# Optimization experiments

Hardware: AMD Instinct MI355X
Metric: run time of the kernel (lower is better)

The kernel has to match this reference:

```python
import jax, jax.numpy as jnp
import numpy as np

B, HW, ENC, DEC, ATTN = 512, 196, 2048, 512, 512

def setup_inputs() -> dict:
    key = jax.random.key(0)
    ks = jax.random.split(key, 8)
    s_enc = 1.0 / np.sqrt(ENC)
    s_dec = 1.0 / np.sqrt(DEC)
    s_v = 1.0 / np.sqrt(ATTN)
    return {
        "enc_out": jax.random.normal(ks[0], (B, HW, ENC), dtype=jnp.float32),
        "dec_h": jax.random.normal(ks[1], (B, DEC), dtype=jnp.float32),
        "W_enc": jax.random.uniform(ks[2], (ENC, ATTN), jnp.float32, -s_enc, s_enc),
        "b_enc": jax.random.uniform(ks[3], (ATTN,), jnp.float32, -s_enc, s_enc),
        "W_dec": jax.random.uniform(ks[4], (DEC, ATTN), jnp.float32, -s_dec, s_dec),
        "b_dec": jax.random.uniform(ks[5], (ATTN,), jnp.float32, -s_dec, s_dec),
        "W_v": jax.random.uniform(ks[6], (ATTN,), jnp.float32, -s_v, s_v),
        "b_v": jax.random.uniform(ks[7], (), jnp.float32, -s_v, s_v),
    }

def reference(enc_out, dec_h, W_enc, b_enc, W_dec, b_dec, W_v, b_v):
    # attn1: [B, HW, ATTN]; attn2: [B, 1, ATTN]
    attn1 = jnp.einsum('bse,ea->bsa', enc_out, W_enc) + b_enc
    attn2 = (dec_h @ W_dec + b_dec)[:, None, :]
    score = jax.nn.relu(attn1 + attn2)
    logits = jnp.einsum('bsa,a->bs', score, W_v) + b_v  # [B, HW]
    alpha = jax.nn.softmax(logits, axis=1)
    context_vec = jnp.einsum('bs,bse->be', alpha, enc_out)
    return (context_vec, alpha)
```

## Files before the change

kernel.cpp:

```cpp
#include <hip/hip_runtime.h>
#include <hip/hip_bf16.h>
#include <cstdint>
#include <cstddef>

#define B_    512
#define HW_   196
#define ENC_  2048
#define DEC_  512
#define ATTN_ 512
#define M_    (B_*HW_)

typedef __attribute__((ext_vector_type(8))) short short8;
typedef __attribute__((ext_vector_type(4))) float f32x4;

__device__ __forceinline__ unsigned short f2bf(float x) {
  __bf16 b = (__bf16)x;
  return __builtin_bit_cast(unsigned short, b);
}
__device__ __forceinline__ unsigned int cvt2(float x, float y) {
  return (unsigned)f2bf(x) | ((unsigned)f2bf(y) << 16);
}

__device__ __forceinline__ void gload_lds16(const void* g, void* l) {
  __builtin_amdgcn_global_load_lds(
      (const __attribute__((address_space(1))) void*)g,
      (__attribute__((address_space(3))) void*)l, 16, 0, 0);
}

__device__ __forceinline__ int invswz8(int p) {
  const int b2 = ((p >> 2) ^ (p >> 4)) & 1;
  const int b1 = ((p >> 1) ^ (p >> 3)) & 1;
  const int b0 = (p ^ (p >> 2) ^ (p >> 4)) & 1;
  return (p & ~7) | (b2 << 2) | (b1 << 1) | b0;
}

__global__ __launch_bounds__(256)
void k_attn2(const float* __restrict__ dec_h, const float* __restrict__ Wdec,
             const float* __restrict__ bdec, const float* __restrict__ benc,
             float* __restrict__ attn2p) {
  __shared__ float dh[DEC_];
  const int b = blockIdx.x;
  const int t = threadIdx.x;
  dh[t]       = dec_h[b*DEC_ + t];
  dh[t + 256] = dec_h[b*DEC_ + t + 256];
  __syncthreads();
  #pragma unroll
  for (int rep = 0; rep < 2; ++rep) {
    const int a = t + rep*256;
    float acc = bdec[a] + benc[a];
    #pragma unroll 8
    for (int k = 0; k < DEC_; ++k)
      acc = fmaf(dh[k], Wdec[(size_t)k*ATTN_ + a], acc);
    attn2p[(size_t)b*ATTN_ + a] = acc;
  }
}

__global__ __launch_bounds__(256)
void k_transpose(const float* __restrict__ Wenc, unsigned short* __restrict__ WencT) {
  __shared__ float tile[32][33];
  const int e0 = blockIdx.x * 32;
  const int a0 = blockIdx.y * 32;
  const int t  = threadIdx.x;
  const int li = t >> 5;
  const int lj = t & 31;
  #pragma unroll
  for (int rep = 0; rep < 4; ++rep) {
    const int i = li + rep*8;
    tile[i][lj] = Wenc[(size_t)(e0 + i)*ATTN_ + a0 + lj];
  }
  __syncthreads();
  #pragma unroll
  for (int rep = 0; rep < 4; ++rep) {
    const int ar = li + rep*8;
    WencT[(size_t)(a0 + ar)*ENC_ + e0 + lj] = f2bf(tile[lj][ar]);
  }
}

#define BM 128
#define BN 128
#define BK 32
#define LDA 40
#define NT (ENC_/BK)

__global__ __launch_bounds__(256)
void k_gemm_logits(const float* __restrict__ enc,
                   const unsigned short* __restrict__ WencT,
                   const float* __restrict__ attn2p,
                   const float* __restrict__ Wv,
                   float* __restrict__ partials) {
  __shared__ unsigned short As[BM*LDA];
  __shared__ unsigned short Bs[2][BN*BK];
  __shared__ float plog[BM][2];

  const int tid  = threadIdx.x;
  const int id   = blockIdx.x;
  const int xcd  = id & 7;
  const int rest = id >> 3;
  const int nb   = rest & 3;
  const int mblk = (rest >> 2) * 8 + xcd;
  const int r0 = mblk * BM;
  const int n0 = nb * BN;

  const int arow  = tid >> 1;
  const int ahalf = (tid & 1) << 4;
  const float* aptr = enc + (size_t)(r0 + arow)*ENC_ + ahalf;

  const unsigned short* bbase = WencT + (size_t)n0*ENC_;

  const int w  = tid >> 6;
  const int l  = tid & 63;
  const int wm = w >> 1, wn = w & 1;
  const int lrow = l & 15;
  const int kg   = l >> 4;
  const int lk8  = kg << 3;
  const int g4   = kg << 2;

  f32x4 acc[4][4];
  #pragma unroll
  for (int mi = 0; mi < 4; ++mi)
    #pragma unroll
    for (int ni = 0; ni < 4; ++ni)
      acc[mi][ni] = (f32x4){0.f, 0.f, 0.f, 0.f};

  float4 ar[4];
  #pragma unroll
  for (int i = 0; i < 4; ++i) ar[i] = *reinterpret_cast<const float4*>(aptr + i*4);
  #pragma unroll
  for (int r = 0; r < 2; ++r) {
    const int p = r*256 + tid;
    const int c = invswz8(p);
    gload_lds16(bbase + (size_t)(c >> 2)*ENC_ + (c & 3)*8, &Bs[0][p*8]);
  }

  for (int kt = 0; kt < NT; ++kt) {
    {
      unsigned int pk[8];
      #pragma unroll
      for (int i = 0; i < 4; ++i) {
        pk[2*i]   = cvt2(ar[i].x, ar[i].y);
        pk[2*i+1] = cvt2(ar[i].z, ar[i].w);
      }
      uint4* da = reinterpret_cast<uint4*>(&As[arow*LDA + ahalf]);
      da[0] = make_uint4(pk[0], pk[1], pk[2], pk[3]);
      da[1] = make_uint4(pk[4], pk[5], pk[6], pk[7]);
    }
    __syncthreads();

    if (kt + 1 < NT) {
      const float* ap = aptr + (kt + 1)*BK;
      #pragma unroll
      for (int i = 0; i < 4; ++i) ar[i] = *reinterpret_cast<const float4*>(ap + i*4);
      const int k0n = (kt + 1)*BK;
      unsigned short* bdst = Bs[(kt + 1) & 1];
      #pragma unroll
      for (int r = 0; r < 2; ++r) {
        const int p = r*256 + tid;
        const int c = invswz8(p);
        gload_lds16(bbase + (size_t)(c >> 2)*ENC_ + k0n + (c & 3)*8, &bdst[p*8]);
      }
    }

    const unsigned short* bsc = Bs[kt & 1];
    short8 aF[4], bF[4];
    #pragma unroll
    for (int mi = 0; mi < 4; ++mi)
      aF[mi] = *reinterpret_cast<const short8*>(&As[(wm*64 + mi*16 + lrow)*LDA + lk8]);
    #pragma unroll
    for (int ni = 0; ni < 4; ++ni) {
      const int cr = ((wn*64 + ni*16 + lrow) << 2) + kg;
      const int pr = cr ^ ((cr >> 2) & 7);
      bF[ni] = *reinterpret_cast<const short8*>(&bsc[pr << 3]);
    }
    #pragma unroll
    for (int mi = 0; mi < 4; ++mi)
      #pragma unroll
      for (int ni = 0; ni < 4; ++ni)
        acc[mi][ni] = __builtin_amdgcn_mfma_f32_16x16x32_bf16(aF[mi], bF[ni], acc[mi][ni], 0, 0, 0);
    __syncthreads();
  }

  float wvv[4];
  #pragma unroll
  for (int ni = 0; ni < 4; ++ni) wvv[ni] = Wv[n0 + wn*64 + ni*16 + lrow];
  #pragma unroll
  for (int mi = 0; mi < 4; ++mi) {
    #pragma unroll
    for (int j = 0; j < 4; ++j) {
      const int row_local = wm*64 + mi*16 + g4 + j;
      const int r  = r0 + row_local;
      const int bb = r / HW_;
      const float* a2 = attn2p + (size_t)bb*ATTN_ + n0 + wn*64;
      float s = 0.f;
      #pragma unroll
      for (int ni = 0; ni < 4; ++ni) {
        float v = acc[mi][ni][j] + a2[ni*16 + lrow];
        v = fmaxf(v, 0.f);
        s = fmaf(v, wvv[ni], s);
      }
      s += __shfl_xor(s, 1);
      s += __shfl_xor(s, 2);
      s += __shfl_xor(s, 4);
      s += __shfl_xor(s, 8);
      if (lrow == 0) plog[row_local][wn] = s;
    }
  }
  __syncthreads();
  if (tid < BM)
    partials[(size_t)(r0 + tid)*4 + nb] = plog[tid][0] + plog[tid][1];
}

__global__ __launch_bounds__(64)
void k_softmax(const float* __restrict__ partials, const float* __restrict__ bvp,
               float* __restrict__ alpha) {
  const int b = blockIdx.x;
  const int t = threadIdx.x;
  const float bv = bvp[0];
  float lg[4];
  #pragma unroll
  for (int i = 0; i < 4; ++i) {
    const int s = t + i*64;
    if (s < HW_) {
      const float4 p = *reinterpret_cast<const float4*>(&partials[(size_t)(b*HW_ + s)*4]);
      lg[i] = p.x + p.y + p.z + p.w + bv;
    } else lg[i] = -INFINITY;
  }
  float mx = fmaxf(fmaxf(lg[0], lg[1]), fmaxf(lg[2], lg[3]));
  #pragma unroll
  for (int off = 32; off; off >>= 1) mx = fmaxf(mx, __shfl_xor(mx, off));
  float sum = 0.f;
  #pragma unroll
  for (int i = 0; i < 4; ++i) { lg[i] = expf(lg[i] - mx); sum += lg[i]; }
  #pragma unroll
  for (int off = 32; off; off >>= 1) sum += __shfl_xor(sum, off);
  const float inv = 1.0f / sum;
  #pragma unroll
  for (int i = 0; i < 4; ++i) {
    const int s = t + i*64;
    if (s < HW_) alpha[b*HW_ + s] = lg[i] * inv;
  }
}

__global__ __launch_bounds__(256)
void k_context(const float* __restrict__ enc, const float* __restrict__ alpha,
               float* __restrict__ ctx) {
  __shared__ float al[HW_];
  const int bi = blockIdx.x;
  const int b  = bi >> 1;
  const int e0 = (bi & 1) << 10;
  const int t  = threadIdx.x;
  if (t < HW_) al[t] = alpha[b*HW_ + t];
  __syncthreads();
  const float* base = enc + (size_t)b*HW_*ENC_ + e0 + t*4;
  float4 acc = {0.f, 0.f, 0.f, 0.f};
  #pragma unroll 4
  for (int s = 0; s < HW_; ++s) {
    const float a = al[s];
    const float4 v = *reinterpret_cast<const float4*>(base + (size_t)s*ENC_);
    acc.x = fmaf(a, v.x, acc.x);
    acc.y = fmaf(a, v.y, acc.y);
    acc.z = fmaf(a, v.z, acc.z);
    acc.w = fmaf(a, v.w, acc.w);
  }
  *reinterpret_cast<float4*>(&ctx[(size_t)b*ENC_ + e0 + t*4]) = acc;
}

extern "C" void kernel_launch(void* const* d_in, const int* in_sizes, int n_in,
                              void* d_out, int out_size, void* d_ws, size_t ws_size,
                              hipStream_t stream) {
  const float* enc   = (const float*)d_in[0];
  const float* dec_h = (const float*)d_in[1];
  const float* Wenc  = (const float*)d_in[2];
  const float* benc  = (const float*)d_in[3];
  const float* Wdec  = (const float*)d_in[4];
  const float* bdec  = (const float*)d_in[5];
  const float* Wv    = (const float*)d_in[6];
  const float* bv    = (const float*)d_in[7];

  float* ctx   = (float*)d_out;
  float* alpha = (float*)d_out + (size_t)B_*ENC_;

  char* ws = (char*)d_ws;
  float*          attn2p   = (float*)ws;
  unsigned short* WencT    = (unsigned short*)(ws + (1u << 20));
  float*          partials = (float*)(ws + 3u*(1u << 20));

  hipLaunchKernelGGL(k_attn2,     dim3(B_),               dim3(256), 0, stream,
                     dec_h, Wdec, bdec, benc, attn2p);
  hipLaunchKernelGGL(k_transpose, dim3(ENC_/32, ATTN_/32), dim3(256), 0, stream,
                     Wenc, WencT);
  hipLaunchKernelGGL(k_gemm_logits, dim3(3136),           dim3(256), 0, stream,
                     enc, WencT, attn2p, Wv, partials);
  hipLaunchKernelGGL(k_softmax,   dim3(B_),               dim3(64),  0, stream,
                     partials, bv, alpha);
  hipLaunchKernelGGL(k_context,   dim3(1024),             dim3(256), 0, stream,
                     enc, alpha, ctx);
}
```

Baseline: 673.3 us.

## Deepen GEMM pipeline with double-buffered A, triple-buffered B, single barrier

Restructures the logits GEMM main loop so the A tile is double-buffered in LDS and B is triple-buffered. Each iteration now uses one barrier instead of two, with a hand-written s_waitcnt. The global loads for A (register prefetch) and B (direct-to-LDS) are issued two k-steps ahead, and the loop is unrolled by two using a macro. The aim is to hide global memory latency and cut synchronization overhead. The cost is more LDS use, which may lower occupancy, and the waitcnt value must correctly account for outstanding loads.

```diff
diff --git a/kernel.cpp b/kernel.cpp
--- a/kernel.cpp
+++ b/kernel.cpp
@@ -88,8 +88,8 @@
                    const float* __restrict__ attn2p,
                    const float* __restrict__ Wv,
                    float* __restrict__ partials) {
-  __shared__ unsigned short As[BM*LDA];
-  __shared__ unsigned short Bs[2][BN*BK];
+  __shared__ unsigned short As[2][BM*LDA];
+  __shared__ unsigned short Bs[3][BN*BK];
   __shared__ float plog[BM][2];
 
   const int tid  = threadIdx.x;
@@ -122,62 +122,86 @@
     for (int ni = 0; ni < 4; ++ni)
       acc[mi][ni] = (f32x4){0.f, 0.f, 0.f, 0.f};
 
-  float4 ar[4];
-  #pragma unroll
-  for (int i = 0; i < 4; ++i) ar[i] = *reinterpret_cast<const float4*>(aptr + i*4);
+  float4 Xa[4], Ya[4];
+  #pragma unroll
+  for (int i = 0; i < 4; ++i) Xa[i] = *reinterpret_cast<const float4*>(aptr + i*4);
   #pragma unroll
   for (int r = 0; r < 2; ++r) {
     const int p = r*256 + tid;
     const int c = invswz8(p);
     gload_lds16(bbase + (size_t)(c >> 2)*ENC_ + (c & 3)*8, &Bs[0][p*8]);
   }
-
-  for (int kt = 0; kt < NT; ++kt) {
-    {
-      unsigned int pk[8];
-      #pragma unroll
-      for (int i = 0; i < 4; ++i) {
-        pk[2*i]   = cvt2(ar[i].x, ar[i].y);
-        pk[2*i+1] = cvt2(ar[i].z, ar[i].w);
-      }
-      uint4* da = reinterpret_cast<uint4*>(&As[arow*LDA + ahalf]);
-      da[0] = make_uint4(pk[0], pk[1], pk[2], pk[3]);
-      da[1] = make_uint4(pk[4], pk[5], pk[6], pk[7]);
-    }
-    __syncthreads();
-
-    if (kt + 1 < NT) {
-      const float* ap = aptr + (kt + 1)*BK;
-      #pragma unroll
-      for (int i = 0; i < 4; ++i) ar[i] = *reinterpret_cast<const float4*>(ap + i*4);
-      const int k0n = (kt + 1)*BK;
-      unsigned short* bdst = Bs[(kt + 1) & 1];
-      #pragma unroll
-      for (int r = 0; r < 2; ++r) {
-        const int p = r*256 + tid;
-        const int c = invswz8(p);
-        gload_lds16(bbase + (size_t)(c >> 2)*ENC_ + k0n + (c & 3)*8, &bdst[p*8]);
-      }
-    }
-
-    const unsigned short* bsc = Bs[kt & 1];
-    short8 aF[4], bF[4];
-    #pragma unroll
-    for (int mi = 0; mi < 4; ++mi)
-      aF[mi] = *reinterpret_cast<const short8*>(&As[(wm*64 + mi*16 + lrow)*LDA + lk8]);
-    #pragma unroll
-    for (int ni = 0; ni < 4; ++ni) {
-      const int cr = ((wn*64 + ni*16 + lrow) << 2) + kg;
-      const int pr = cr ^ ((cr >> 2) & 7);
-      bF[ni] = *reinterpret_cast<const short8*>(&bsc[pr << 3]);
-    }
-    #pragma unroll
-    for (int mi = 0; mi < 4; ++mi)
-      #pragma unroll
-      for (int ni = 0; ni < 4; ++ni)
-        acc[mi][ni] = __builtin_amdgcn_mfma_f32_16x16x32_bf16(aF[mi], bF[ni], acc[mi][ni], 0, 0, 0);
-    __syncthreads();
-  }
+  #pragma unroll
+  for (int i = 0; i < 4; ++i) Ya[i] = *reinterpret_cast<const float4*>(aptr + BK + i*4);
+  #pragma unroll
+  for (int r = 0; r < 2; ++r) {
+    const int p = r*256 + tid;
+    const int c = invswz8(p);
+    gload_lds16(bbase + (size_t)(c >> 2)*ENC_ + BK + (c & 3)*8, &Bs[1][p*8]);
+  }
+
+  int bcur = 0;
+
+#define STEP(SA, KT) do {                                                      \
+                                    \
+    uint4 pk0, pk1;                                                            \
+    pk0.x = cvt2(SA[0].x, SA[0].y);  pk0.y = cvt2(SA[0].z, SA[0].w);           \
+    pk0.z = cvt2(SA[1].x, SA[1].y);  pk0.w = cvt2(SA[1].z, SA[1].w);           \
+    pk1.x = cvt2(SA[2].x, SA[2].y);  pk1.y = cvt2(SA[2].z, SA[2].w);           \
+    pk1.z = cvt2(SA[3].x, SA[3].y);  pk1.w = cvt2(SA[3].z, SA[3].w);           \
+    {                                                                          \
+      uint4* da = reinterpret_cast<uint4*>(&As[(KT) & 1][arow*LDA + ahalf]);   \
+      da[0] = pk0; da[1] = pk1;                                                \
+    }                                                                          \
+    if ((KT) + 2 < NT) {                           \
+      const float* ap = aptr + ((KT) + 2)*BK;                                  \
+      _Pragma("unroll")                                                        \
+      for (int i = 0; i < 4; ++i)                                              \
+        SA[i] = *reinterpret_cast<const float4*>(ap + i*4);                    \
+    }                                                                          \
+      \
+    asm volatile("s_waitcnt vmcnt(10) lgkmcnt(0)" ::: "memory");               \
+    __builtin_amdgcn_s_barrier();                                              \
+    asm volatile("" ::: "memory");                                             \
+    if ((KT) + 2 < NT) {  \
+      unsigned short* bdst = &Bs[bcur >= 1 ? bcur - 1 : 2][0];                 \
+      const int k0n = ((KT) + 2)*BK;                                           \
+      _Pragma("unroll")                                                        \
+      for (int r = 0; r < 2; ++r) {                                            \
+        const int p = r*256 + tid;                                             \
+        const int c = invswz8(p);                                              \
+        gload_lds16(bbase + (size_t)(c >> 2)*ENC_ + k0n + (c & 3)*8, &bdst[p*8]); \
+      }                                                                        \
+    }                                                                          \
+                                                          \
+    {                                                                          \
+      const unsigned short* asrc = &As[(KT) & 1][0];                           \
+      const unsigned short* bsc  = &Bs[bcur][0];                               \
+      short8 aF[4], bF[4];                                                     \
+      _Pragma("unroll")                                                        \
+      for (int mi = 0; mi < 4; ++mi)                                           \
+        aF[mi] = *reinterpret_cast<const short8*>(&asrc[(wm*64 + mi*16 + lrow)*LDA + lk8]); \
+      _Pragma("unroll")                                                        \
+      for (int ni = 0; ni < 4; ++ni) {                                         \
+        const int cr = ((wn*64 + ni*16 + lrow) << 2) + kg;                     \
+        const int pr = cr ^ ((cr >> 2) & 7);                                   \
+        bF[ni] = *reinterpret_cast<const short8*>(&bsc[pr << 3]);              \
+      }                                                                        \
+      _Pragma("unroll")                                                        \
+      for (int mi = 0; mi < 4; ++mi)                                           \
+        _Pragma("unroll")                                                      \
+        for (int ni = 0; ni < 4; ++ni)                                         \
+          acc[mi][ni] = __builtin_amdgcn_mfma_f32_16x16x32_bf16(               \
+              aF[mi], bF[ni], acc[mi][ni], 0, 0, 0);                           \
+    }                                                                          \
+    bcur = (bcur == 2) ? 0 : bcur + 1;                                         \
+  } while (0)
+
+  for (int kt = 0; kt < NT; kt += 2) {
+    STEP(Xa, kt);
+    STEP(Ya, kt + 1);
+  }
+#undef STEP
 
   float wvv[4];
   #pragma unroll
@@ -284,14 +308,14 @@
   unsigned short* WencT    = (unsigned short*)(ws + (1u << 20));
   float*          partials = (float*)(ws + 3u*(1u << 20));
 
-  hipLaunchKernelGGL(k_attn2,     dim3(B_),               dim3(256), 0, stream,
+  hipLaunchKernelGGL(k_attn2,     dim3(B_),                dim3(256), 0, stream,
                      dec_h, Wdec, bdec, benc, attn2p);
   hipLaunchKernelGGL(k_transpose, dim3(ENC_/32, ATTN_/32), dim3(256), 0, stream,
                      Wenc, WencT);
-  hipLaunchKernelGGL(k_gemm_logits, dim3(3136),           dim3(256), 0, stream,
+  hipLaunchKernelGGL(k_gemm_logits, dim3(3136),            dim3(256), 0, stream,
                      enc, WencT, attn2p, Wv, partials);
-  hipLaunchKernelGGL(k_softmax,   dim3(B_),               dim3(64),  0, stream,
+  hipLaunchKernelGGL(k_softmax,   dim3(B_),                dim3(64),  0, stream,
                      partials, bv, alpha);
-  hipLaunchKernelGGL(k_context,   dim3(1024),             dim3(256), 0, stream,
+  hipLaunchKernelGGL(k_context,   dim3(1024),              dim3(256), 0, stream,
                      enc, alpha, ctx);
 }
```

After: 738.5 us. 9.7% more time.

## Stream fp32 A tiles via direct global-to-LDS loads with double buffering

Applied to the files above, without the earlier changes.

The GEMM no longer loads fp32 encoder rows into registers and converts them to bf16 before an LDS store. A tiles now go straight from global memory into double-buffered fp32 LDS with an XOR swizzle, using async global_load_lds like the B tiles. Conversion to bf16 happens when fragments are read from LDS. The main loop is unrolled by two so the buffer index is static, and one barrier per step is dropped. This doubles A's LDS footprint, which may reduce occupancy, and adds conversion work in the MFMA-feeding path.

```diff
diff --git a/kernel.cpp b/kernel.cpp
--- a/kernel.cpp
+++ b/kernel.cpp
@@ -79,7 +79,6 @@
 #define BM 128
 #define BN 128
 #define BK 32
-#define LDA 40
 #define NT (ENC_/BK)
 
 __global__ __launch_bounds__(256)
@@ -88,7 +87,7 @@
                    const float* __restrict__ attn2p,
                    const float* __restrict__ Wv,
                    float* __restrict__ partials) {
-  __shared__ unsigned short As[BM*LDA];
+  __shared__ float          Asf[2][BM*BK];
   __shared__ unsigned short Bs[2][BN*BK];
   __shared__ float plog[BM][2];
 
@@ -101,19 +100,47 @@
   const int r0 = mblk * BM;
   const int n0 = nb * BN;
 
-  const int arow  = tid >> 1;
-  const int ahalf = (tid & 1) << 4;
-  const float* aptr = enc + (size_t)(r0 + arow)*ENC_ + ahalf;
-
-  const unsigned short* bbase = WencT + (size_t)n0*ENC_;
-
   const int w  = tid >> 6;
   const int l  = tid & 63;
   const int wm = w >> 1, wn = w & 1;
   const int lrow = l & 15;
   const int kg   = l >> 4;
-  const int lk8  = kg << 3;
   const int g4   = kg << 2;
+
+  int   aQ[4];
+  const float* aSrc[4];
+  #pragma unroll
+  for (int j = 0; j < 4; ++j) {
+    const int Q   = w*256 + j*64 + l;
+    const int row = Q >> 3;
+    const int cc  = Q & 7;
+    aQ[j]   = Q;
+    aSrc[j] = enc + (size_t)(r0 + row)*ENC_ + (size_t)((cc ^ (row & 7)) << 2);
+  }
+  int   bPp[2];
+  const unsigned short* bSrc[2];
+  #pragma unroll
+  for (int r = 0; r < 2; ++r) {
+    const int p = r*256 + tid;
+    const int c = invswz8(p);
+    bPp[r]  = p;
+    bSrc[r] = WencT + (size_t)(n0 + (c >> 2))*ENC_ + (size_t)((c & 3) << 3);
+  }
+
+  int aOff[4][2];
+  #pragma unroll
+  for (int mi = 0; mi < 4; ++mi) {
+    const int R = wm*64 + mi*16 + lrow;
+    aOff[mi][0] = R*BK + (((2*kg)     ^ (R & 7)) << 2);
+    aOff[mi][1] = R*BK + (((2*kg + 1) ^ (R & 7)) << 2);
+  }
+  int bOff[4];
+  #pragma unroll
+  for (int ni = 0; ni < 4; ++ni) {
+    const int cr = ((wn*64 + ni*16 + lrow) << 2) + kg;
+    const int pr = cr ^ ((cr >> 2) & 7);
+    bOff[ni] = pr << 3;
+  }
 
   f32x4 acc[4][4];
   #pragma unroll
@@ -122,62 +149,56 @@
     for (int ni = 0; ni < 4; ++ni)
       acc[mi][ni] = (f32x4){0.f, 0.f, 0.f, 0.f};
 
-  float4 ar[4];
-  #pragma unroll
-  for (int i = 0; i < 4; ++i) ar[i] = *reinterpret_cast<const float4*>(aptr + i*4);
-  #pragma unroll
-  for (int r = 0; r < 2; ++r) {
-    const int p = r*256 + tid;
-    const int c = invswz8(p);
-    gload_lds16(bbase + (size_t)(c >> 2)*ENC_ + (c & 3)*8, &Bs[0][p*8]);
-  }
-
-  for (int kt = 0; kt < NT; ++kt) {
-    {
-      unsigned int pk[8];
-      #pragma unroll
-      for (int i = 0; i < 4; ++i) {
-        pk[2*i]   = cvt2(ar[i].x, ar[i].y);
-        pk[2*i+1] = cvt2(ar[i].z, ar[i].w);
-      }
-      uint4* da = reinterpret_cast<uint4*>(&As[arow*LDA + ahalf]);
-      da[0] = make_uint4(pk[0], pk[1], pk[2], pk[3]);
-      da[1] = make_uint4(pk[4], pk[5], pk[6], pk[7]);
-    }
-    __syncthreads();
-
-    if (kt + 1 < NT) {
-      const float* ap = aptr + (kt + 1)*BK;
-      #pragma unroll
-      for (int i = 0; i < 4; ++i) ar[i] = *reinterpret_cast<const float4*>(ap + i*4);
-      const int k0n = (kt + 1)*BK;
-      unsigned short* bdst = Bs[(kt + 1) & 1];
-      #pragma unroll
-      for (int r = 0; r < 2; ++r) {
-        const int p = r*256 + tid;
-        const int c = invswz8(p);
-        gload_lds16(bbase + (size_t)(c >> 2)*ENC_ + k0n + (c & 3)*8, &bdst[p*8]);
-      }
-    }
-
-    const unsigned short* bsc = Bs[kt & 1];
-    short8 aF[4], bF[4];
-    #pragma unroll
-    for (int mi = 0; mi < 4; ++mi)
-      aF[mi] = *reinterpret_cast<const short8*>(&As[(wm*64 + mi*16 + lrow)*LDA + lk8]);
-    #pragma unroll
-    for (int ni = 0; ni < 4; ++ni) {
-      const int cr = ((wn*64 + ni*16 + lrow) << 2) + kg;
-      const int pr = cr ^ ((cr >> 2) & 7);
-      bF[ni] = *reinterpret_cast<const short8*>(&bsc[pr << 3]);
-    }
-    #pragma unroll
-    for (int mi = 0; mi < 4; ++mi)
-      #pragma unroll
-      for (int ni = 0; ni < 4; ++ni)
-        acc[mi][ni] = __builtin_amdgcn_mfma_f32_16x16x32_bf16(aF[mi], bF[ni], acc[mi][ni], 0, 0, 0);
-    __syncthreads();
-  }
+  #pragma unroll
+  for (int j = 0; j < 4; ++j) gload_lds16(aSrc[j], &Asf[0][aQ[j] << 2]);
+  #pragma unroll
+  for (int r = 0; r < 2; ++r) gload_lds16(bSrc[r], &Bs[0][bPp[r] << 3]);
+  #pragma unroll
+  for (int j = 0; j < 4; ++j) aSrc[j] += BK;
+  #pragma unroll
+  for (int r = 0; r < 2; ++r) bSrc[r] += BK;
+  __syncthreads();
+
+#define STEP(P, COND) do {                                                     \
+    if (COND) {                             \
+      _Pragma("unroll")                                                        \
+      for (int j = 0; j < 4; ++j) {                                            \
+        gload_lds16(aSrc[j], &Asf[(P)^1][aQ[j] << 2]);                         \
+        aSrc[j] += BK;                                                         \
+      }                                                                        \
+      _Pragma("unroll")                                                        \
+      for (int r = 0; r < 2; ++r) {                                            \
+        gload_lds16(bSrc[r], &Bs[(P)^1][bPp[r] << 3]);                         \
+        bSrc[r] += BK;                                                         \
+      }                                                                        \
+    }                                                                          \
+    short8 aF[4], bF[4];                                                       \
+    _Pragma("unroll")                                                          \
+    for (int mi = 0; mi < 4; ++mi) {                                           \
+      const f32x4 a0 = *reinterpret_cast<const f32x4*>(&Asf[P][aOff[mi][0]]);  \
+      const f32x4 a1 = *reinterpret_cast<const f32x4*>(&Asf[P][aOff[mi][1]]);  \
+      uint4 pk;                                                                \
+      pk.x = cvt2(a0.x, a0.y);  pk.y = cvt2(a0.z, a0.w);                       \
+      pk.z = cvt2(a1.x, a1.y);  pk.w = cvt2(a1.z, a1.w);                       \
+      aF[mi] = __builtin_bit_cast(short8, pk);                                 \
+    }                                                                          \
+    _Pragma("unroll")                                                          \
+    for (int ni = 0; ni < 4; ++ni)                                             \
+      bF[ni] = *reinterpret_cast<const short8*>(&Bs[P][bOff[ni]]);             \
+    _Pragma("unroll")                                                          \
+    for (int mi = 0; mi < 4; ++mi)                                             \
+      _Pragma("unroll")                                                        \
+      for (int ni = 0; ni < 4; ++ni)                                           \
+        acc[mi][ni] = __builtin_amdgcn_mfma_f32_16x16x32_bf16(                 \
+            aF[mi], bF[ni], acc[mi][ni], 0, 0, 0);                             \
+    __syncthreads();                        \
+  } while (0)
+
+  for (int kt = 0; kt < NT; kt += 2) {
+    STEP(0, true);
+    STEP(1, kt + 2 < NT);
+  }
+#undef STEP
 
   float wvv[4];
   #pragma unroll
@@ -284,14 +305,14 @@
   unsigned short* WencT    = (unsigned short*)(ws + (1u << 20));
   float*          partials = (float*)(ws + 3u*(1u << 20));
 
-  hipLaunchKernelGGL(k_attn2,     dim3(B_),               dim3(256), 0, stream,
+  hipLaunchKernelGGL(k_attn2,     dim3(B_),                dim3(256), 0, stream,
                      dec_h, Wdec, bdec, benc, attn2p);
   hipLaunchKernelGGL(k_transpose, dim3(ENC_/32, ATTN_/32), dim3(256), 0, stream,
                      Wenc, WencT);
-  hipLaunchKernelGGL(k_gemm_logits, dim3(3136),           dim3(256), 0, stream,
+  hipLaunchKernelGGL(k_gemm_logits, dim3(3136),            dim3(256), 0, stream,
                      enc, WencT, attn2p, Wv, partials);
-  hipLaunchKernelGGL(k_softmax,   dim3(B_),               dim3(64),  0, stream,
+  hipLaunchKernelGGL(k_softmax,   dim3(B_),                dim3(64),  0, stream,
                      partials, bv, alpha);
-  hipLaunchKernelGGL(k_context,   dim3(1024),             dim3(256), 0, stream,
+  hipLaunchKernelGGL(k_context,   dim3(1024),              dim3(256), 0, stream,
                      enc, alpha, ctx);
 }
```

New measurement: 772.1 us. 14.7% more time.

## Pre-convert encoder output to bf16 and use it in GEMM and context

Applied to the files above, without the earlier changes.

Adds a pass that converts the whole fp32 encoder output into a bf16 copy in workspace. The GEMM then streams bf16 A tiles straight into LDS with swizzled async loads and double buffering, with no per-tile conversion, and the context reduction reads the bf16 copy. This is meant to halve the A-operand traffic in the GEMM and the context kernel, paid for by one extra full read and write of the encoder output. It also changes numerics: the context is now computed from bf16 values, and a workspace-size check falls back to the old path.

```diff
diff --git a/kernel.cpp b/kernel.cpp
--- a/kernel.cpp
+++ b/kernel.cpp
@@ -32,6 +32,20 @@
   const int b1 = ((p >> 1) ^ (p >> 3)) & 1;
   const int b0 = (p ^ (p >> 2) ^ (p >> 4)) & 1;
   return (p & ~7) | (b2 << 2) | (b1 << 1) | b0;
+}
+
+__global__ __launch_bounds__(256)
+void k_convert(const float* __restrict__ in, unsigned short* __restrict__ out) {
+  const size_t total  = (size_t)M_ * ENC_;
+  const size_t stride = (size_t)gridDim.x * 256 * 8;
+  for (size_t i = ((size_t)blockIdx.x * 256 + threadIdx.x) * 8; i < total; i += stride) {
+    const float4 a = *reinterpret_cast<const float4*>(in + i);
+    const float4 b = *reinterpret_cast<const float4*>(in + i + 4);
+    uint4 o;
+    o.x = cvt2(a.x, a.y);  o.y = cvt2(a.z, a.w);
+    o.z = cvt2(b.x, b.y);  o.w = cvt2(b.z, b.w);
+    *reinterpret_cast<uint4*>(out + i) = o;
+  }
 }
 
 __global__ __launch_bounds__(256)
@@ -79,16 +93,15 @@
 #define BM 128
 #define BN 128
 #define BK 32
-#define LDA 40
 #define NT (ENC_/BK)
 
 __global__ __launch_bounds__(256)
-void k_gemm_logits(const float* __restrict__ enc,
-                   const unsigned short* __restrict__ WencT,
-                   const float* __restrict__ attn2p,
-                   const float* __restrict__ Wv,
-                   float* __restrict__ partials) {
-  __shared__ unsigned short As[BM*LDA];
+void k_gemm_logits_bf16(const unsigned short* __restrict__ ench,
+                        const unsigned short* __restrict__ WencT,
+                        const float* __restrict__ attn2p,
+                        const float* __restrict__ Wv,
+                        float* __restrict__ partials) {
+  __shared__ unsigned short As[2][BM*BK];
   __shared__ unsigned short Bs[2][BN*BK];
   __shared__ float plog[BM][2];
 
@@ -101,83 +114,83 @@
   const int r0 = mblk * BM;
   const int n0 = nb * BN;
 
-  const int arow  = tid >> 1;
-  const int ahalf = (tid & 1) << 4;
-  const float* aptr = enc + (size_t)(r0 + arow)*ENC_ + ahalf;
-
-  const unsigned short* bbase = WencT + (size_t)n0*ENC_;
-
   const int w  = tid >> 6;
   const int l  = tid & 63;
   const int wm = w >> 1, wn = w & 1;
   const int lrow = l & 15;
   const int kg   = l >> 4;
-  const int lk8  = kg << 3;
   const int g4   = kg << 2;
 
-  f32x4 acc[4][4];
-  #pragma unroll
-  for (int mi = 0; mi < 4; ++mi)
-    #pragma unroll
-    for (int ni = 0; ni < 4; ++ni)
-      acc[mi][ni] = (f32x4){0.f, 0.f, 0.f, 0.f};
-
-  float4 ar[4];
-  #pragma unroll
-  for (int i = 0; i < 4; ++i) ar[i] = *reinterpret_cast<const float4*>(aptr + i*4);
+  int pp[2];
+  const unsigned short* aSrc[2];
+  const unsigned short* bSrc[2];
   #pragma unroll
   for (int r = 0; r < 2; ++r) {
     const int p = r*256 + tid;
     const int c = invswz8(p);
-    gload_lds16(bbase + (size_t)(c >> 2)*ENC_ + (c & 3)*8, &Bs[0][p*8]);
-  }
-
-  for (int kt = 0; kt < NT; ++kt) {
-    {
-      unsigned int pk[8];
-      #pragma unroll
-      for (int i = 0; i < 4; ++i) {
-        pk[2*i]   = cvt2(ar[i].x, ar[i].y);
-        pk[2*i+1] = cvt2(ar[i].z, ar[i].w);
-      }
-      uint4* da = reinterpret_cast<uint4*>(&As[arow*LDA + ahalf]);
-      da[0] = make_uint4(pk[0], pk[1], pk[2], pk[3]);
-      da[1] = make_uint4(pk[4], pk[5], pk[6], pk[7]);
-    }
-    __syncthreads();
-
-    if (kt + 1 < NT) {
-      const float* ap = aptr + (kt + 1)*BK;
-      #pragma unroll
-      for (int i = 0; i < 4; ++i) ar[i] = *reinterpret_cast<const float4*>(ap + i*4);
-      const int k0n = (kt + 1)*BK;
-      unsigned short* bdst = Bs[(kt + 1) & 1];
-      #pragma unroll
-      for (int r = 0; r < 2; ++r) {
-        const int p = r*256 + tid;
-        const int c = invswz8(p);
-        gload_lds16(bbase + (size_t)(c >> 2)*ENC_ + k0n + (c & 3)*8, &bdst[p*8]);
-      }
-    }
-
-    const unsigned short* bsc = Bs[kt & 1];
-    short8 aF[4], bF[4];
-    #pragma unroll
-    for (int mi = 0; mi < 4; ++mi)
-      aF[mi] = *reinterpret_cast<const short8*>(&As[(wm*64 + mi*16 + lrow)*LDA + lk8]);
-    #pragma unroll
-    for (int ni = 0; ni < 4; ++ni) {
-      const int cr = ((wn*64 + ni*16 + lrow) << 2) + kg;
-      const int pr = cr ^ ((cr >> 2) & 7);
-      bF[ni] = *reinterpret_cast<const short8*>(&bsc[pr << 3]);
-    }
-    #pragma unroll
-    for (int mi = 0; mi < 4; ++mi)
-      #pragma unroll
-      for (int ni = 0; ni < 4; ++ni)
-        acc[mi][ni] = __builtin_amdgcn_mfma_f32_16x16x32_bf16(aF[mi], bF[ni], acc[mi][ni], 0, 0, 0);
-    __syncthreads();
-  }
+    const int row = c >> 2, cj = c & 3;
+    pp[r]   = p;
+    aSrc[r] = ench  + (size_t)(r0 + row)*ENC_ + (size_t)(cj << 3);
+    bSrc[r] = WencT + (size_t)(n0 + row)*ENC_ + (size_t)(cj << 3);
+  }
+
+  int aOff[4], bOff[4];
+  #pragma unroll
+  for (int mi = 0; mi < 4; ++mi) {
+    const int cr = ((wm*64 + mi*16 + lrow) << 2) + kg;
+    aOff[mi] = (cr ^ ((cr >> 2) & 7)) << 3;
+  }
+  #pragma unroll
+  for (int ni = 0; ni < 4; ++ni) {
+    const int cr = ((wn*64 + ni*16 + lrow) << 2) + kg;
+    bOff[ni] = (cr ^ ((cr >> 2) & 7)) << 3;
+  }
+
+  f32x4 acc[4][4];
+  #pragma unroll
+  for (int mi = 0; mi < 4; ++mi)
+    #pragma unroll
+    for (int ni = 0; ni < 4; ++ni)
+      acc[mi][ni] = (f32x4){0.f, 0.f, 0.f, 0.f};
+
+  #pragma unroll
+  for (int r = 0; r < 2; ++r) {
+    gload_lds16(aSrc[r], &As[0][pp[r] << 3]);
+    gload_lds16(bSrc[r], &Bs[0][pp[r] << 3]);
+    aSrc[r] += BK;  bSrc[r] += BK;
+  }
+  __syncthreads();
+
+#define STEP(P, COND) do {                                                     \
+    if (COND) {                                                                \
+      _Pragma("unroll")                                                        \
+      for (int r = 0; r < 2; ++r) {                                            \
+        gload_lds16(aSrc[r], &As[(P)^1][pp[r] << 3]);                          \
+        gload_lds16(bSrc[r], &Bs[(P)^1][pp[r] << 3]);                          \
+        aSrc[r] += BK;  bSrc[r] += BK;                                         \
+      }                                                                        \
+    }                                                                          \
+    short8 aF[4], bF[4];                                                       \
+    _Pragma("unroll")                                                          \
+    for (int mi = 0; mi < 4; ++mi)                                             \
+      aF[mi] = *reinterpret_cast<const short8*>(&As[P][aOff[mi]]);             \
+    _Pragma("unroll")                                                          \
+    for (int ni = 0; ni < 4; ++ni)                                             \
+      bF[ni] = *reinterpret_cast<const short8*>(&Bs[P][bOff[ni]]);             \
+    _Pragma("unroll")                                                          \
+    for (int mi = 0; mi < 4; ++mi)                                             \
+      _Pragma("unroll")                                                        \
+      for (int ni = 0; ni < 4; ++ni)                                           \
+        acc[mi][ni] = __builtin_amdgcn_mfma_f32_16x16x32_bf16(                 \
+            aF[mi], bF[ni], acc[mi][ni], 0, 0, 0);                             \
+    __syncthreads();                                                           \
+  } while (0)
+
+  for (int kt = 0; kt < NT; kt += 2) {
+    STEP(0, true);
+    STEP(1, kt + 2 < NT);
+  }
+#undef STEP
 
   float wvv[4];
   #pragma unroll
@@ -209,6 +222,131 @@
     partials[(size_t)(r0 + tid)*4 + nb] = plog[tid][0] + plog[tid][1];
 }
 
+#define LDA 40
+__global__ __launch_bounds__(256)
+void k_gemm_logits_f32(const float* __restrict__ enc,
+                       const unsigned short* __restrict__ WencT,
+                       const float* __restrict__ attn2p,
+                       const float* __restrict__ Wv,
+                       float* __restrict__ partials) {
+  __shared__ unsigned short As[BM*LDA];
+  __shared__ unsigned short Bs[2][BN*BK];
+  __shared__ float plog[BM][2];
+
+  const int tid  = threadIdx.x;
+  const int id   = blockIdx.x;
+  const int xcd  = id & 7;
+  const int rest = id >> 3;
+  const int nb   = rest & 3;
+  const int mblk = (rest >> 2) * 8 + xcd;
+  const int r0 = mblk * BM;
+  const int n0 = nb * BN;
+
+  const int arow  = tid >> 1;
+  const int ahalf = (tid & 1) << 4;
+  const float* aptr = enc + (size_t)(r0 + arow)*ENC_ + ahalf;
+  const unsigned short* bbase = WencT + (size_t)n0*ENC_;
+
+  const int w  = tid >> 6;
+  const int l  = tid & 63;
+  const int wm = w >> 1, wn = w & 1;
+  const int lrow = l & 15;
+  const int kg   = l >> 4;
+  const int lk8  = kg << 3;
+  const int g4   = kg << 2;
+
+  f32x4 acc[4][4];
+  #pragma unroll
+  for (int mi = 0; mi < 4; ++mi)
+    #pragma unroll
+    for (int ni = 0; ni < 4; ++ni)
+      acc[mi][ni] = (f32x4){0.f, 0.f, 0.f, 0.f};
+
+  float4 ar[4];
+  #pragma unroll
+  for (int i = 0; i < 4; ++i) ar[i] = *reinterpret_cast<const float4*>(aptr + i*4);
+  #pragma unroll
+  for (int r = 0; r < 2; ++r) {
+    const int p = r*256 + tid;
+    const int c = invswz8(p);
+    gload_lds16(bbase + (size_t)(c >> 2)*ENC_ + (c & 3)*8, &Bs[0][p*8]);
+  }
+
+  for (int kt = 0; kt < NT; ++kt) {
+    {
+      unsigned int pk[8];
+      #pragma unroll
+      for (int i = 0; i < 4; ++i) {
+        pk[2*i]   = cvt2(ar[i].x, ar[i].y);
+        pk[2*i+1] = cvt2(ar[i].z, ar[i].w);
+      }
+      uint4* da = reinterpret_cast<uint4*>(&As[arow*LDA + ahalf]);
+      da[0] = make_uint4(pk[0], pk[1], pk[2], pk[3]);
+      da[1] = make_uint4(pk[4], pk[5], pk[6], pk[7]);
+    }
+    __syncthreads();
+    if (kt + 1 < NT) {
+      const float* ap = aptr + (kt + 1)*BK;
+      #pragma unroll
+      for (int i = 0; i < 4; ++i) ar[i] = *reinterpret_cast<const float4*>(ap + i*4);
+      const int k0n = (kt + 1)*BK;
+      unsigned short* bdst = Bs[(kt + 1) & 1];
+      #pragma unroll
+      for (int r = 0; r < 2; ++r) {
+        const int p = r*256 + tid;
+        const int c = invswz8(p);
+        gload_lds16(bbase + (size_t)(c >> 2)*ENC_ + k0n + (c & 3)*8, &bdst[p*8]);
+      }
+    }
+    const unsigned short* bsc = Bs[kt & 1];
+    short8 aF[4], bF[4];
+    #pragma unroll
+    for (int mi = 0; mi < 4; ++mi)
+      aF[mi] = *reinterpret_cast<const short8*>(&As[(wm*64 + mi*16 + lrow)*LDA + lk8]);
+    #pragma unroll
+    for (int ni = 0; ni < 4; ++ni) {
+      const int cr = ((wn*64 + ni*16 + lrow) << 2) + kg;
+      const int pr = cr ^ ((cr >> 2) & 7);
+      bF[ni] = *reinterpret_cast<const short8*>(&bsc[pr << 3]);
+    }
+    #pragma unroll
+    for (int mi = 0; mi < 4; ++mi)
+      #pragma unroll
+      for (int ni = 0; ni < 4; ++ni)
+        acc[mi][ni] = __builtin_amdgcn_mfma_f32_16x16x32_bf16(aF[mi], bF[ni], acc[mi][ni], 0, 0, 0);
+    __syncthreads();
+  }
+
+  float wvv[4];
+  #pragma unroll
+  for (int ni = 0; ni < 4; ++ni) wvv[ni] = Wv[n0 + wn*64 + ni*16 + lrow];
+  #pragma unroll
+  for (int mi = 0; mi < 4; ++mi) {
+    #pragma unroll
+    for (int j = 0; j < 4; ++j) {
+      const int row_local = wm*64 + mi*16 + g4 + j;
+      const int r  = r0 + row_local;
+      const int bb = r / HW_;
+      const float* a2 = attn2p + (size_t)bb*ATTN_ + n0 + wn*64;
+      float s = 0.f;
+      #pragma unroll
+      for (int ni = 0; ni < 4; ++ni) {
+        float v = acc[mi][ni][j] + a2[ni*16 + lrow];
+        v = fmaxf(v, 0.f);
+        s = fmaf(v, wvv[ni], s);
+      }
+      s += __shfl_xor(s, 1);
+      s += __shfl_xor(s, 2);
+      s += __shfl_xor(s, 4);
+      s += __shfl_xor(s, 8);
+      if (lrow == 0) plog[row_local][wn] = s;
+    }
+  }
+  __syncthreads();
+  if (tid < BM)
+    partials[(size_t)(r0 + tid)*4 + nb] = plog[tid][0] + plog[tid][1];
+}
+
 __global__ __launch_bounds__(64)
 void k_softmax(const float* __restrict__ partials, const float* __restrict__ bvp,
                float* __restrict__ alpha) {
@@ -241,8 +379,36 @@
 }
 
 __global__ __launch_bounds__(256)
-void k_context(const float* __restrict__ enc, const float* __restrict__ alpha,
-               float* __restrict__ ctx) {
+void k_context_bf16(const unsigned short* __restrict__ ench,
+                    const float* __restrict__ alpha, float* __restrict__ ctx) {
+  __shared__ float al[HW_];
+  const int b = blockIdx.x;
+  const int t = threadIdx.x;
+  if (t < HW_) al[t] = alpha[b*HW_ + t];
+  __syncthreads();
+  const unsigned short* base = ench + (size_t)b*HW_*ENC_ + t*8;
+  float acc[8] = {0.f,0.f,0.f,0.f,0.f,0.f,0.f,0.f};
+  #pragma unroll 2
+  for (int s = 0; s < HW_; ++s) {
+    const uint4 v = *reinterpret_cast<const uint4*>(base + (size_t)s*ENC_);
+    const float a = al[s];
+    const unsigned u[4] = {v.x, v.y, v.z, v.w};
+    #pragma unroll
+    for (int q = 0; q < 4; ++q) {
+      const float lo = __builtin_bit_cast(float, u[q] << 16);
+      const float hi = __builtin_bit_cast(float, u[q] & 0xffff0000u);
+      acc[2*q]   = fmaf(a, lo, acc[2*q]);
+      acc[2*q+1] = fmaf(a, hi, acc[2*q+1]);
+    }
+  }
+  float4* o = reinterpret_cast<float4*>(&ctx[(size_t)b*ENC_ + t*8]);
+  o[0] = make_float4(acc[0], acc[1], acc[2], acc[3]);
+  o[1] = make_float4(acc[4], acc[5], acc[6], acc[7]);
+}
+
+__global__ __launch_bounds__(256)
+void k_context_f32(const float* __restrict__ enc, const float* __restrict__ alpha,
+                   float* __restrict__ ctx) {
   __shared__ float al[HW_];
   const int bi = blockIdx.x;
   const int b  = bi >> 1;
@@ -283,15 +449,29 @@
   float*          attn2p   = (float*)ws;
   unsigned short* WencT    = (unsigned short*)(ws + (1u << 20));
   float*          partials = (float*)(ws + 3u*(1u << 20));
-
-  hipLaunchKernelGGL(k_attn2,     dim3(B_),               dim3(256), 0, stream,
+  unsigned short* ench     = (unsigned short*)(ws + 5u*(1u << 20));
+  const size_t needed = 5u*(1u << 20) + (size_t)M_*ENC_*sizeof(unsigned short);
+  const bool big = (ws_size >= needed);
+
+  hipLaunchKernelGGL(k_attn2,     dim3(B_),                dim3(256), 0, stream,
                      dec_h, Wdec, bdec, benc, attn2p);
   hipLaunchKernelGGL(k_transpose, dim3(ENC_/32, ATTN_/32), dim3(256), 0, stream,
                      Wenc, WencT);
-  hipLaunchKernelGGL(k_gemm_logits, dim3(3136),           dim3(256), 0, stream,
-                     enc, WencT, attn2p, Wv, partials);
-  hipLaunchKernelGGL(k_softmax,   dim3(B_),               dim3(64),  0, stream,
-                     partials, bv, alpha);
-  hipLaunchKernelGGL(k_context,   dim3(1024),             dim3(256), 0, stream,
-                     enc, alpha, ctx);
-}
+  if (big) {
+    hipLaunchKernelGGL(k_convert,   dim3(2048),            dim3(256), 0, stream,
+                       enc, ench);
+    hipLaunchKernelGGL(k_gemm_logits_bf16, dim3(3136),     dim3(256), 0, stream,
+                       ench, WencT, attn2p, Wv, partials);
+    hipLaunchKernelGGL(k_softmax,   dim3(B_),              dim3(64),  0, stream,
+                       partials, bv, alpha);
+    hipLaunchKernelGGL(k_context_bf16, dim3(B_),           dim3(256), 0, stream,
+                       ench, alpha, ctx);
+  } else {
+    hipLaunchKernelGGL(k_gemm_logits_f32, dim3(3136),      dim3(256), 0, stream,
+                       enc, WencT, attn2p, Wv, partials);
+    hipLaunchKernelGGL(k_softmax,   dim3(B_),              dim3(64),  0, stream,
+                       partials, bv, alpha);
+    hipLaunchKernelGGL(k_context_f32, dim3(1024),          dim3(256), 0, stream,
+                       enc, alpha, ctx);
+  }
+}
```

New measurement: 803.4 us. 1.19x slower.
